# Kernel optimization log

Hardware: AMD Instinct MI355X
Metric: run time of the kernel (lower is better)

Reference implementation:

```python
import jax, jax.numpy as jnp
import numpy as np

B, T, D = 2, 2048, 2048
N, K, H = 16, 8, 128  # num_heads, num_kv_heads, head_dim
SOFTCAP = 50.0
ROPE_BASE = 10000.0


def apply_rope(x, positions):
    # x: [B, L, heads, H], positions: [B, L]
    head_dim = x.shape[-1]
    fraction = 2.0 * jnp.arange(head_dim // 2, dtype=jnp.float32) / head_dim
    timescale = ROPE_BASE ** fraction  # [H/2]
    sinusoid = positions.astype(jnp.float32)[..., None] / timescale  # [B, L, H/2]
    sinusoid = sinusoid[..., None, :]  # [B, L, 1, H/2]
    sin, cos = jnp.sin(sinusoid), jnp.cos(sinusoid)
    first, second = jnp.split(x, 2, axis=-1)
    out = jnp.concatenate([first * cos - second * sin,
                           second * cos + first * sin], axis=-1)
    return out.astype(x.dtype)


def setup_inputs() -> dict:
    key = jax.random.key(0)
    kx, kq, kkv, ko = jax.random.split(key, 4)
    x = jax.random.normal(kx, (B, T, D), dtype=jnp.float32)
    positions = jnp.broadcast_to(jnp.arange(T, dtype=jnp.int32), (B, T))
    attn_mask = jnp.broadcast_to(
        jnp.tril(jnp.ones((T, T), dtype=bool))[None, None], (B, 1, T, T))
    # variance-scaling fan_in init approximated with scaled normals
    w_q = jax.random.normal(kq, (N, D, H), dtype=jnp.float32) / np.sqrt(D)
    w_kv = jax.random.normal(kkv, (2, K, D, H), dtype=jnp.float32) / np.sqrt(D)
    w_out = jax.random.normal(ko, (N, H, D), dtype=jnp.float32) / np.sqrt(N * H)
    return {"x": x, "positions": positions, "attn_mask": attn_mask,
            "w_q": w_q, "w_kv": w_kv, "w_out": w_out}


def reference(x, positions, attn_mask, w_q, w_kv, w_out):
    # QKV projections (GQA: separate q and kv einsums)
    q = jnp.einsum('BTD,NDH->BTNH', x, w_q)        # [B,T,N,H]
    kv = jnp.einsum('BSD,cKDH->cBSKH', x, w_kv)     # [2,B,S,K,H]
    k, v = kv[0], kv[1]
    q = apply_rope(q, positions) * (H ** -0.5)      # rsqrt_head_dim norm
    k = apply_rope(k, positions)
    # GQA grouping: N = K * G
    G = N // K
    qg = q.reshape(B, T, K, G, H)
    logits = jnp.einsum('BTKGH,BSKH->BKGTS', qg, k).astype(jnp.float32)
    logits = jnp.tanh(logits / SOFTCAP) * SOFTCAP   # logits softcap
    big_neg = -2.3819763e+38
    masked = jnp.where(attn_mask[:, :, None, :, :], logits, big_neg)
    probs = jax.nn.softmax(masked, axis=-1).astype(k.dtype)
    encoded = jnp.einsum('BKGTS,BSKH->BTKGH', probs, v).reshape(B, T, N, H)
    return jnp.einsum('BTNH,NHD->BTD', encoded, w_out)
```

## Files before the change

kernel.cpp:

```cpp
#include <hip/hip_runtime.h>
#include <math.h>
#include <stdint.h>


typedef unsigned short u16;
using bf16x8 = __attribute__((ext_vector_type(8))) short;
using f32x4  = __attribute__((ext_vector_type(4))) float;

#define MFMA_BF16(a,b,c) __builtin_amdgcn_mfma_f32_16x16x32_bf16((a),(b),(c),0,0,0)

static __device__ __forceinline__ float b2f(u16 u) {
  union { unsigned int i; float f; } v; v.i = ((unsigned int)u) << 16; return v.f;
}
static __device__ __forceinline__ u16 f2b(float f) {
  union { float f; unsigned int i; } v; v.f = f;
  unsigned int r = v.i + 0x7fffu + ((v.i >> 16) & 1u);
  return (u16)(r >> 16);
}
static __device__ __forceinline__ unsigned pk2(float x0, float x1) {
  union { float f; unsigned u; } a, b;
  a.f = x0; b.f = x1;
  return __builtin_amdgcn_perm(b.u + 0x8000u, a.u + 0x8000u, 0x07060302u);
}
static __device__ __forceinline__ void gload_lds16(const void* g, void* l) {
  __builtin_amdgcn_global_load_lds((__attribute__((address_space(1))) void*)(g),
                                   (__attribute__((address_space(3))) void*)(l),
                                   16, 0, 0);
}

__global__ __launch_bounds__(256) void prep(const float* __restrict__ x, u16* __restrict__ xb,
                                            const float* __restrict__ wq,
                                            const float* __restrict__ wkv,
                                            const float* __restrict__ wout,
                                            u16* __restrict__ wqkvt, u16* __restrict__ woutt) {
  const int tid = threadIdx.x;
  int bid = blockIdx.x;
  if (bid < 8192) {
    const int i = (bid * 256 + tid) * 4;
    const float4 v = *(const float4*)(x + i);
    ushort4 o;
    o.x = f2b(v.x); o.y = f2b(v.y); o.z = f2b(v.z); o.w = f2b(v.w);
    *(ushort4*)(xb + i) = o;
    return;
  }
  bid -= 8192;
  const float* src;
  u16* dst;
  int rows, cols, bx, by;
  if (bid < 8192) {
    const int seg = bid >> 12;
    const int r = bid & 4095;
    const int mat = r >> 8;
    bx = (r & 255) & 3;
    by = (r & 255) >> 2;
    rows = 2048; cols = 128;
    src = (seg ? wkv : wq) + (size_t)mat * 2048 * 128;
    dst = wqkvt + (size_t)(seg * 16 + mat) * 2048 * 128;
  } else {
    const int r = bid - 8192;
    bx = r & 63;
    by = r >> 6;
    rows = 2048; cols = 2048;
    src = wout;
    dst = woutt;
  }
  __shared__ u16 tile[32][33];
  const int c0 = bx * 32, r0 = by * 32;
  const int tx = tid & 31, ty = tid >> 5;
#pragma unroll
  for (int j = 0; j < 4; ++j)
    tile[ty + j * 8][tx] = f2b(src[(size_t)(r0 + ty + j * 8) * cols + (c0 + tx)]);
  __syncthreads();
#pragma unroll
  for (int j = 0; j < 4; ++j)
    dst[(size_t)(c0 + ty + j * 8) * rows + (r0 + tx)] = tile[tx][ty + j * 8];
}

__global__ __launch_bounds__(256) void gemm_qkv(const u16* __restrict__ X,
                                                const u16* __restrict__ wqkvt,
                                                u16* __restrict__ qb,
                                                u16* __restrict__ kb,
                                                u16* __restrict__ vtb) {
  __shared__ __align__(16) u16 sA[128 * 64];
  __shared__ __align__(16) u16 sB[128 * 64];
  const int m0 = blockIdx.x * 128;
  const int ct = blockIdx.y;
  const u16* Bt = wqkvt + (size_t)ct * 128 * 2048;
  const int tid = threadIdx.x;
  const int wave = tid >> 6, lane = tid & 63;
  const int wm = wave & 1, wn = wave >> 1;
  const int quad = lane >> 4, l16 = lane & 15;
  const int srow = lane >> 3;
  const int sch = (lane & 7) ^ srow;

  f32x4 acc[4][4] = {};

  for (int k0 = 0; k0 < 2048; k0 += 64) {
#pragma unroll
    for (int s = 0; s < 4; ++s) {
      const int instr = wave * 4 + s;
      const int row = instr * 8 + srow;
      gload_lds16(X + (size_t)(m0 + row) * 2048 + k0 + sch * 8, (char*)sA + instr * 1024);
      gload_lds16(Bt + (size_t)row * 2048 + k0 + sch * 8, (char*)sB + instr * 1024);
    }
    __syncthreads();
#pragma unroll
    for (int ks = 0; ks < 2; ++ks) {
      bf16x8 af[4], bfr[4];
#pragma unroll
      for (int mf = 0; mf < 4; ++mf) {
        const int R = wm * 64 + mf * 16 + l16;
        af[mf] = *(const bf16x8*)((char*)sA + R * 128 + (((ks * 4 + quad) ^ (R & 7)) << 4));
      }
#pragma unroll
      for (int nf = 0; nf < 4; ++nf) {
        const int R = wn * 64 + nf * 16 + l16;
        bfr[nf] = *(const bf16x8*)((char*)sB + R * 128 + (((ks * 4 + quad) ^ (R & 7)) << 4));
      }
#pragma unroll
      for (int mf = 0; mf < 4; ++mf)
#pragma unroll
        for (int nf = 0; nf < 4; ++nf)
          acc[mf][nf] = MFMA_BF16(af[mf], bfr[nf], acc[mf][nf]);
    }
    __syncthreads();
  }

#pragma unroll
  for (int mf = 0; mf < 4; ++mf) {
    const int mm = m0 + wm * 64 + mf * 16 + quad * 4;
    const int b = mm >> 11;
    const int t = mm & 2047;
#pragma unroll
    for (int nf = 0; nf < 4; ++nf) {
      const int h = wn * 64 + nf * 16 + l16;
      if (ct < 16) {
        u16* d = qb + (((size_t)b * 16 + ct) * 2048 + t) * 128 + h;
#pragma unroll
        for (int i = 0; i < 4; ++i) d[(size_t)i * 128] = f2b(acc[mf][nf][i]);
      } else if (ct < 24) {
        u16* d = kb + (((size_t)b * 8 + (ct - 16)) * 2048 + t) * 128 + h;
#pragma unroll
        for (int i = 0; i < 4; ++i) d[(size_t)i * 128] = f2b(acc[mf][nf][i]);
      } else {
        u16* d = vtb + (((size_t)b * 8 + (ct - 24)) * 128 + h) * 2048 + t;
        uint2 pkv;
        pkv.x = (unsigned)f2b(acc[mf][nf][0]) | ((unsigned)f2b(acc[mf][nf][1]) << 16);
        pkv.y = (unsigned)f2b(acc[mf][nf][2]) | ((unsigned)f2b(acc[mf][nf][3]) << 16);
        *(uint2*)d = pkv;
      }
    }
  }
}

__global__ __launch_bounds__(256) void rope_kernel(u16* __restrict__ qb,
                                                   u16* __restrict__ kb,
                                                   const int* __restrict__ pos) {
  const unsigned idx = blockIdx.x * 256 + threadIdx.x;
  const unsigned QP = 1u << 21;
  u16* p;
  float scale;
  int b, t, j2;
  if (idx < QP) {
    j2 = (int)(idx & 31) * 2; t = (int)((idx >> 5) & 2047);
    const int hd = (int)((idx >> 16) & 15); b = (int)(idx >> 20);
    p = qb + (((size_t)b * 16 + hd) * 2048 + t) * 128;
    scale = 0.08838834764831845f;
  } else {
    const unsigned r = idx - QP;
    j2 = (int)(r & 31) * 2; t = (int)((r >> 5) & 2047);
    const int hd = (int)((r >> 16) & 7); b = (int)(r >> 19);
    p = kb + (((size_t)b * 8 + hd) * 2048 + t) * 128;
    scale = 1.0f;
  }
  const float fpos = (float)pos[(size_t)b * 2048 + t];
  const unsigned lo = *(const unsigned*)(p + j2);
  const unsigned hi = *(const unsigned*)(p + j2 + 64);
  unsigned olo = 0, ohi = 0;
#pragma unroll
  for (int d = 0; d < 2; ++d) {
    const int j = j2 + d;
    const float ts = __powf(10000.0f, (float)j * (1.0f / 64.0f));
    float sn, cs;
    sincosf(fpos / ts, &sn, &cs);
    const float a = b2f((u16)((d ? (lo >> 16) : lo) & 0xffffu));
    const float c2 = b2f((u16)((d ? (hi >> 16) : hi) & 0xffffu));
    olo |= ((unsigned)f2b((a * cs - c2 * sn) * scale)) << (16 * d);
    ohi |= ((unsigned)f2b((c2 * cs + a * sn) * scale)) << (16 * d);
  }
  *(unsigned*)(p + j2) = olo;
  *(unsigned*)(p + j2 + 64) = ohi;
}

__global__ __launch_bounds__(256, 4) void attn_fused(const u16* __restrict__ qg,
                                                     const u16* __restrict__ kg,
                                                     const u16* __restrict__ vtg,
                                                     u16* __restrict__ enc) {
  __shared__ __align__(16) char lds[32768];
  char* sK = lds;
  char* sV = lds + 16384;

  const int bid = blockIdx.x;
  const int half = bid >> 9;
  const int r = bid & 511;
  const int x = r & 7;
  const int g = r >> 3;
  const int pr = g & 15;
  const int head = (g >> 4) * 8 + x;
  const int Q = half ? pr : (31 - pr);
  const int b = head >> 4;
  const int n = head & 15;
  const int kh = n >> 1;

  const u16* qbase = qg + ((size_t)b * 16 + n) * 2048 * 128;
  const u16* kbase = kg + ((size_t)b * 8 + kh) * 2048 * 128;
  const u16* vbase = vtg + ((size_t)b * 8 + kh) * 128 * 2048;

  const int tid = threadIdx.x, wave = tid >> 6, lane = tid & 63;
  const int quad = lane >> 4, l16 = lane & 15;
  const int bp_a0 = ((quad & 1) * 32 + l16) * 4;
  const int bp_a1 = bp_a0 + 64;

  const float L2E = 1.4426950408889634f;
  const float C50 = 72.13475204444817f;
  const float A1 = 1.3333333333e-4f;
  const float A2 = 2.1333333333e-8f;
  const float A3 = 3.4539682540e-12f;

  const u16* kp[4];
  const u16* vp[4];
#pragma unroll
  for (int s = 0; s < 4; ++s) {
    const int kr = wave * 16 + s * 4 + quad;
    kp[s] = kbase + (size_t)kr * 128 + (l16 ^ (s * 4 + quad)) * 8;
    const int vr = wave * 32 + s * 8 + (lane >> 3);
    vp[s] = vbase + (size_t)vr * 2048 + ((lane & 7) ^ (lane >> 3)) * 8;
  }

  const int tw = Q * 64 + wave * 16;
  const int tlane = tw + l16;

  bf16x8 qf[4];
#pragma unroll
  for (int kf = 0; kf < 4; ++kf)
    qf[kf] = *(const bf16x8*)(qbase + (size_t)tlane * 128 + kf * 32 + quad * 8);

  f32x4 o[8] = {};
  f32x4 lacc = {0.f, 0.f, 0.f, 0.f};

#pragma unroll 1
  for (int si = 0; si <= Q; ++si) {
    const int s0 = si * 64;
    __syncthreads();
#pragma unroll
    for (int s = 0; s < 4; ++s) {
      gload_lds16(kp[s], sK + (wave * 4 + s) * 1024);
      gload_lds16(vp[s], sV + (wave * 4 + s) * 1024);
      kp[s] += 64 * 128;
      vp[s] += 64;
    }
    __syncthreads();

    const bool diag = (si == Q);
    const int nfmax = diag ? wave : 3;
    const int kmax = diag ? (wave >> 1) : 1;

    f32x4 sacc[4];
#pragma unroll
    for (int nf = 0; nf < 4; ++nf) {
      if (nf <= nfmax) {
        const int sr = nf * 16 + l16;
        f32x4 a = {0.f, 0.f, 0.f, 0.f};
#pragma unroll
        for (int kf = 0; kf < 4; ++kf) {
          const bf16x8 kfr =
              *(const bf16x8*)(sK + sr * 256 + (((kf * 4 + quad) ^ (sr & 15)) << 4));
          a = MFMA_BF16(kfr, qf[kf], a);
        }
        sacc[nf] = a;
      }
    }

#pragma unroll
    for (int nf = 0; nf < 4; ++nf) {
      if (nf <= nfmax) {
        const f32x4 xv = sacc[nf];
        const f32x4 u = xv * xv;
        f32x4 t = u * (-A3) + A2;
        t = u * t + (-A1);
        t = u * t + 1.0f;
        const f32x4 tc = xv * t;
        f32x4 pv;
#pragma unroll
        for (int i = 0; i < 4; ++i) pv[i] = exp2f(fmaf(tc[i], L2E, -C50));
        if (diag) {
#pragma unroll
          for (int i = 0; i < 4; ++i) {
            const int sg = s0 + nf * 16 + quad * 4 + i;
            if (sg > tlane) pv[i] = 0.0f;
          }
        }
        sacc[nf] = pv;
        lacc += pv;
      }
    }

    unsigned pkd[4][2];
#pragma unroll
    for (int nf = 0; nf < 4; ++nf) {
      if (nf <= nfmax) {
        pkd[nf][0] = pk2(sacc[nf][0], sacc[nf][1]);
        pkd[nf][1] = pk2(sacc[nf][2], sacc[nf][3]);
      } else {
        pkd[nf][0] = 0u; pkd[nf][1] = 0u;
      }
    }

#pragma unroll
    for (int c2 = 0; c2 < 2; ++c2) {
      if (c2 <= kmax) {
        const int lo = (quad >> 1);
        const int dA0 = __builtin_amdgcn_ds_bpermute(bp_a0, (int)pkd[2 * c2][0]);
        const int dB0 = __builtin_amdgcn_ds_bpermute(bp_a0, (int)pkd[2 * c2 + 1][0]);
        const int dA1 = __builtin_amdgcn_ds_bpermute(bp_a0, (int)pkd[2 * c2][1]);
        const int dB1 = __builtin_amdgcn_ds_bpermute(bp_a0, (int)pkd[2 * c2 + 1][1]);
        const int dA2 = __builtin_amdgcn_ds_bpermute(bp_a1, (int)pkd[2 * c2][0]);
        const int dB2 = __builtin_amdgcn_ds_bpermute(bp_a1, (int)pkd[2 * c2 + 1][0]);
        const int dA3 = __builtin_amdgcn_ds_bpermute(bp_a1, (int)pkd[2 * c2][1]);
        const int dB3 = __builtin_amdgcn_ds_bpermute(bp_a1, (int)pkd[2 * c2 + 1][1]);
        union { int d[4]; bf16x8 v; } pb;
        pb.d[0] = lo ? dB0 : dA0;
        pb.d[1] = lo ? dB1 : dA1;
        pb.d[2] = lo ? dB2 : dA2;
        pb.d[3] = lo ? dB3 : dA3;
#pragma unroll
        for (int nfo = 0; nfo < 8; ++nfo) {
          const int hr = nfo * 16 + l16;
          const bf16x8 vb =
              *(const bf16x8*)(sV + hr * 128 + (((c2 * 4 + quad) ^ (hr & 7)) << 4));
          o[nfo] = MFMA_BF16(vb, pb.v, o[nfo]);
        }
      }
    }
  }

  float lsum = lacc[0] + lacc[1] + lacc[2] + lacc[3];
  lsum += __shfl_xor(lsum, 16);
  lsum += __shfl_xor(lsum, 32);
  const float inv = 1.0f / lsum;
  u16* d = enc + (((size_t)b * 2048 + tlane) * 16 + n) * 128 + quad * 4;
#pragma unroll
  for (int nfo = 0; nfo < 8; ++nfo) {
    uint2 st;
    st.x = (unsigned)f2b(o[nfo][0] * inv) | ((unsigned)f2b(o[nfo][1] * inv) << 16);
    st.y = (unsigned)f2b(o[nfo][2] * inv) | ((unsigned)f2b(o[nfo][3] * inv) << 16);
    *(uint2*)(d + nfo * 16) = st;
  }
}

__global__ __launch_bounds__(256) void gemm_out(const u16* __restrict__ A,
                                                const u16* __restrict__ Bt,
                                                float* __restrict__ C) {
  __shared__ __align__(16) u16 sA[128 * 64];
  __shared__ __align__(16) u16 sB[128 * 64];
  const int m0 = blockIdx.x * 128;
  const int n0 = blockIdx.y * 128;
  const int tid = threadIdx.x;
  const int wave = tid >> 6, lane = tid & 63;
  const int wm = wave & 1, wn = wave >> 1;
  const int quad = lane >> 4, l16 = lane & 15;
  const int srow = lane >> 3;
  const int sch = (lane & 7) ^ srow;

  f32x4 acc[4][4] = {};

  for (int k0 = 0; k0 < 2048; k0 += 64) {
#pragma unroll
    for (int s = 0; s < 4; ++s) {
      const int instr = wave * 4 + s;
      const int row = instr * 8 + srow;
      gload_lds16(A + (size_t)(m0 + row) * 2048 + k0 + sch * 8, (char*)sA + instr * 1024);
      gload_lds16(Bt + (size_t)(n0 + row) * 2048 + k0 + sch * 8, (char*)sB + instr * 1024);
    }
    __syncthreads();
#pragma unroll
    for (int ks = 0; ks < 2; ++ks) {
      bf16x8 af[4], bfr[4];
#pragma unroll
      for (int mf = 0; mf < 4; ++mf) {
        const int R = wm * 64 + mf * 16 + l16;
        af[mf] = *(const bf16x8*)((char*)sA + R * 128 + (((ks * 4 + quad) ^ (R & 7)) << 4));
      }
#pragma unroll
      for (int nf = 0; nf < 4; ++nf) {
        const int R = wn * 64 + nf * 16 + l16;
        bfr[nf] = *(const bf16x8*)((char*)sB + R * 128 + (((ks * 4 + quad) ^ (R & 7)) << 4));
      }
#pragma unroll
      for (int mf = 0; mf < 4; ++mf)
#pragma unroll
        for (int nf = 0; nf < 4; ++nf)
          acc[mf][nf] = MFMA_BF16(af[mf], bfr[nf], acc[mf][nf]);
    }
    __syncthreads();
  }

#pragma unroll
  for (int mf = 0; mf < 4; ++mf) {
    const int mm = m0 + wm * 64 + mf * 16 + quad * 4;
#pragma unroll
    for (int nf = 0; nf < 4; ++nf) {
      const int col = n0 + wn * 64 + nf * 16 + l16;
#pragma unroll
      for (int i = 0; i < 4; ++i) C[(size_t)(mm + i) * 2048 + col] = acc[mf][nf][i];
    }
  }
}

extern "C" void kernel_launch(void* const* d_in, const int* in_sizes, int n_in,
                              void* d_out, int out_size, void* d_ws, size_t ws_size,
                              hipStream_t stream) {
  (void)in_sizes; (void)n_in; (void)out_size; (void)ws_size;
  const float* x     = (const float*)d_in[0];
  const int*   posi  = (const int*)d_in[1];
  const float* w_q   = (const float*)d_in[3];
  const float* w_kv  = (const float*)d_in[4];
  const float* w_out = (const float*)d_in[5];
  float* out = (float*)d_out;

  u16* ws = (u16*)d_ws;
  u16* wqkvt = ws;
  u16* woutt = ws + (size_t)8388608;
  u16* qb    = ws + (size_t)12582912;
  u16* kb    = ws + (size_t)20971520;
  u16* vtb   = ws + (size_t)25165824;
  u16* encb  = ws + (size_t)29360128;
  u16* xb    = encb;

  prep<<<20480, 256, 0, stream>>>(x, xb, w_q, w_kv, w_out, wqkvt, woutt);
  gemm_qkv<<<dim3(32, 32), 256, 0, stream>>>(xb, wqkvt, qb, kb, vtb);
  rope_kernel<<<12288, 256, 0, stream>>>(qb, kb, posi);
  attn_fused<<<1024, 256, 0, stream>>>(qb, kb, vtb, encb);
  gemm_out<<<dim3(32, 16), 256, 0, stream>>>(encb, woutt, out);
}
```

Baseline: 402.6 us.

## Enlarge QKV GEMM tile to 256x256 with double-buffered async LDS pipeline

```diff
diff --git a/kernel.cpp b/kernel.cpp
--- a/kernel.cpp
+++ b/kernel.cpp
@@ -76,64 +76,88 @@
     dst[(size_t)(c0 + ty + j * 8) * rows + (r0 + tx)] = tile[tx][ty + j * 8];
 }
 
-__global__ __launch_bounds__(256) void gemm_qkv(const u16* __restrict__ X,
-                                                const u16* __restrict__ wqkvt,
-                                                u16* __restrict__ qb,
-                                                u16* __restrict__ kb,
-                                                u16* __restrict__ vtb) {
-  __shared__ __align__(16) u16 sA[128 * 64];
-  __shared__ __align__(16) u16 sB[128 * 64];
-  const int m0 = blockIdx.x * 128;
-  const int ct = blockIdx.y;
-  const u16* Bt = wqkvt + (size_t)ct * 128 * 2048;
+__global__ __launch_bounds__(512, 2) void gemm_qkv(const u16* __restrict__ X,
+                                                   const u16* __restrict__ wqkvt,
+                                                   u16* __restrict__ qb,
+                                                   u16* __restrict__ kb,
+                                                   u16* __restrict__ vtb) {
+  __shared__ __align__(16) u16 sAB[2][2][16384];
+  const int m0 = blockIdx.x * 256;
+  const int ct0 = blockIdx.y * 2;
+  const u16* BT = wqkvt + (size_t)blockIdx.y * 256 * 2048;
   const int tid = threadIdx.x;
   const int wave = tid >> 6, lane = tid & 63;
-  const int wm = wave & 1, wn = wave >> 1;
+  const int wm = wave >> 2, wn = wave & 3;
   const int quad = lane >> 4, l16 = lane & 15;
   const int srow = lane >> 3;
   const int sch = (lane & 7) ^ srow;
 
-  f32x4 acc[4][4] = {};
-
-  for (int k0 = 0; k0 < 2048; k0 += 64) {
+  f32x4 acc[8][4] = {};
+
+  auto STAGE = [&](int kt, int bsel) {
+    const int k0 = kt * 64;
 #pragma unroll
     for (int s = 0; s < 4; ++s) {
-      const int instr = wave * 4 + s;
-      const int row = instr * 8 + srow;
-      gload_lds16(X + (size_t)(m0 + row) * 2048 + k0 + sch * 8, (char*)sA + instr * 1024);
-      gload_lds16(Bt + (size_t)row * 2048 + k0 + sch * 8, (char*)sB + instr * 1024);
-    }
-    __syncthreads();
+      const int ia = wave * 4 + s;
+      const int row = ia * 8 + srow;
+      gload_lds16(X + (size_t)(m0 + row) * 2048 + k0 + sch * 8,
+                  (char*)&sAB[bsel][0][0] + ia * 1024);
+      gload_lds16(BT + (size_t)row * 2048 + k0 + sch * 8,
+                  (char*)&sAB[bsel][1][0] + ia * 1024);
+    }
+  };
+
+  auto COMPUTE = [&](int bsel) {
+    const char* aB = (const char*)&sAB[bsel][0][0];
+    const char* bB = (const char*)&sAB[bsel][1][0];
 #pragma unroll
     for (int ks = 0; ks < 2; ++ks) {
-      bf16x8 af[4], bfr[4];
-#pragma unroll
-      for (int mf = 0; mf < 4; ++mf) {
-        const int R = wm * 64 + mf * 16 + l16;
-        af[mf] = *(const bf16x8*)((char*)sA + R * 128 + (((ks * 4 + quad) ^ (R & 7)) << 4));
-      }
+      bf16x8 bfr[4];
 #pragma unroll
       for (int nf = 0; nf < 4; ++nf) {
-        const int R = wn * 64 + nf * 16 + l16;
-        bfr[nf] = *(const bf16x8*)((char*)sB + R * 128 + (((ks * 4 + quad) ^ (R & 7)) << 4));
-      }
-#pragma unroll
-      for (int mf = 0; mf < 4; ++mf)
+        const int Rb = wn * 64 + nf * 16 + l16;
+        bfr[nf] = *(const bf16x8*)(bB + Rb * 128 + (((ks * 4 + quad) ^ (Rb & 7)) << 4));
+      }
+      __builtin_amdgcn_s_setprio(1);
+#pragma unroll
+      for (int mf = 0; mf < 8; ++mf) {
+        const int R = wm * 128 + mf * 16 + l16;
+        const bf16x8 af = *(const bf16x8*)(aB + R * 128 + (((ks * 4 + quad) ^ (R & 7)) << 4));
 #pragma unroll
         for (int nf = 0; nf < 4; ++nf)
-          acc[mf][nf] = MFMA_BF16(af[mf], bfr[nf], acc[mf][nf]);
-    }
-    __syncthreads();
-  }
-
-#pragma unroll
-  for (int mf = 0; mf < 4; ++mf) {
-    const int mm = m0 + wm * 64 + mf * 16 + quad * 4;
+          acc[mf][nf] = MFMA_BF16(af, bfr[nf], acc[mf][nf]);
+      }
+      __builtin_amdgcn_s_setprio(0);
+    }
+  };
+
+  STAGE(0, 0);
+#pragma unroll 1
+  for (int t = 0; t < 31; ++t) {
+    STAGE(t + 1, (t + 1) & 1);
+    asm volatile("s_waitcnt vmcnt(8)" ::: "memory");
+    __builtin_amdgcn_s_barrier();
+    asm volatile("" ::: "memory");
+    COMPUTE(t & 1);
+    asm volatile("" ::: "memory");
+    __builtin_amdgcn_s_barrier();
+    asm volatile("" ::: "memory");
+  }
+  asm volatile("s_waitcnt vmcnt(0)" ::: "memory");
+  __builtin_amdgcn_s_barrier();
+  asm volatile("" ::: "memory");
+  COMPUTE(1);
+
+#pragma unroll
+  for (int mf = 0; mf < 8; ++mf) {
+    const int mm = m0 + wm * 128 + mf * 16 + quad * 4;
     const int b = mm >> 11;
     const int t = mm & 2047;
 #pragma unroll
     for (int nf = 0; nf < 4; ++nf) {
-      const int h = wn * 64 + nf * 16 + l16;
+      const int colg = wn * 64 + nf * 16;
+      const int ct = ct0 + (colg >> 7);
+      const int h = (colg & 127) + l16;
       if (ct < 16) {
         u16* d = qb + (((size_t)b * 16 + ct) * 2048 + t) * 128 + h;
 #pragma unroll
@@ -438,7 +462,7 @@
   u16* xb    = encb;
 
   prep<<<20480, 256, 0, stream>>>(x, xb, w_q, w_kv, w_out, wqkvt, woutt);
-  gemm_qkv<<<dim3(32, 32), 256, 0, stream>>>(xb, wqkvt, qb, kb, vtb);
+  gemm_qkv<<<dim3(16, 16), 512, 0, stream>>>(xb, wqkvt, qb, kb, vtb);
   rope_kernel<<<12288, 256, 0, stream>>>(qb, kb, posi);
   attn_fused<<<1024, 256, 0, stream>>>(qb, kb, vtb, encb);
   gemm_out<<<dim3(32, 16), 256, 0, stream>>>(encb, woutt, out);
```

Result: faster. 361.1 us (-10.3%).
